# Kernel optimization log

Measured on AMD Instinct MI355X. Metric: run time of the kernel, lower is better.

## Reference

```python
import jax, jax.numpy as jnp
import numpy as np
from functools import partial

P = 14          # patch size
IMG = 448       # image size
D = 1152        # hidden dim
H = 16          # num heads
DH = D // H     # head dim = 72
I = 4304        # intermediate dim
L = 4           # num layers
N = (IMG // P) ** 2  # 1024 patches
EPS = 1e-6


def setup_inputs() -> dict:
    key = jax.random.key(0)
    ks = jax.random.split(key, 24)
    s = 0.02
    inp = {
        "images": jax.random.normal(ks[0], (2, 2, IMG, IMG, 3), jnp.float32),
        "conv_w": jax.random.normal(ks[1], (P, P, 3, D), jnp.float32) * s,
        "conv_b": jnp.zeros((D,), jnp.float32),
        "pos_emb": jax.random.normal(ks[2], (N, D), jnp.float32) * s,
        # per-layer stacked parameters, leading axis L
        "ln1_g": jnp.ones((L, D), jnp.float32),
        "ln1_b": jnp.zeros((L, D), jnp.float32),
        "Wq": jax.random.normal(ks[3], (L, D, D), jnp.float32) * s,
        "bq": jnp.zeros((L, D), jnp.float32),
        "Wk": jax.random.normal(ks[4], (L, D, D), jnp.float32) * s,
        "bk": jnp.zeros((L, D), jnp.float32),
        "Wv": jax.random.normal(ks[5], (L, D, D), jnp.float32) * s,
        "bv": jnp.zeros((L, D), jnp.float32),
        "Wo": jax.random.normal(ks[6], (L, D, D), jnp.float32) * s,
        "bo": jnp.zeros((L, D), jnp.float32),
        "ln2_g": jnp.ones((L, D), jnp.float32),
        "ln2_b": jnp.zeros((L, D), jnp.float32),
        "W1": jax.random.normal(ks[7], (L, D, I), jnp.float32) * s,
        "b1": jnp.zeros((L, I), jnp.float32),
        "W2": jax.random.normal(ks[8], (L, I, D), jnp.float32) * s,
        "b2": jnp.zeros((L, D), jnp.float32),
        "lnf_g": jnp.ones((D,), jnp.float32),
        "lnf_b": jnp.zeros((D,), jnp.float32),
    }
    return inp


def _layernorm(x, g, b):
    mu = jnp.mean(x, axis=-1, keepdims=True)
    var = jnp.var(x, axis=-1, keepdims=True)
    return (x - mu) * jax.lax.rsqrt(var + EPS) * g + b


def _encoder(images, conv_w, conv_b, pos_emb, ln1_g, ln1_b, Wq, bq, Wk, bk,
             Wv, bv, Wo, bo, ln2_g, ln2_b, W1, b1, W2, b2, lnf_g, lnf_b):
    B, T = images.shape[0], images.shape[1]
    x = images.reshape((B * T,) + images.shape[2:])  # [BT, IMG, IMG, 3]
    # patch embedding: Conv2D stride=kernel=patch, VALID
    x = jax.lax.conv_general_dilated(
        x, conv_w, window_strides=(P, P), padding='VALID',
        dimension_numbers=('NHWC', 'HWIO', 'NHWC')) + conv_b
    x = x.reshape(B * T, N, D) + pos_emb  # add position embedding

    scale = 1.0 / jnp.sqrt(jnp.asarray(DH, x.dtype))

    def block(x, p):
        (g1, b1_, wq, bq_, wk, bk_, wv, bv_, wo, bo_, g2, b2_,
         w1, bm1, w2, bm2) = p
        h = _layernorm(x, g1, b1_)
        q = (h @ wq + bq_).reshape(-1, N, H, DH).transpose(0, 2, 1, 3)
        k = (h @ wk + bk_).reshape(-1, N, H, DH).transpose(0, 2, 1, 3)
        v = (h @ wv + bv_).reshape(-1, N, H, DH).transpose(0, 2, 1, 3)
        scores = jnp.einsum('bhqd,bhkd->bhqk', q, k) * scale
        probs = jax.nn.softmax(scores, axis=-1)
        attn = jnp.einsum('bhqk,bhkd->bhqd', probs, v)
        attn = attn.transpose(0, 2, 1, 3).reshape(-1, N, D)
        x = x + (attn @ wo + bo_)
        h = _layernorm(x, g2, b2_)
        h = jax.nn.gelu(h @ w1 + bm1, approximate=True) @ w2 + bm2
        return x + h, None

    params = (ln1_g, ln1_b, Wq, bq, Wk, bk, Wv, bv, Wo, bo,
              ln2_g, ln2_b, W1, b1, W2, b2)
    x, _ = jax.lax.scan(block, x, params)
    x = _layernorm(x, lnf_g, lnf_b)
    return x.reshape(B, T, N, D)


def reference(images, conv_w, conv_b, pos_emb, ln1_g, ln1_b, Wq, bq, Wk, bk,
              Wv, bv, Wo, bo, ln2_g, ln2_b, W1, b1, W2, b2, lnf_g, lnf_b):
    return _encoder(images, conv_w, conv_b, pos_emb, ln1_g, ln1_b, Wq, bq,
                    Wk, bk, Wv, bv, Wo, bo, ln2_g, ln2_b, W1, b1, W2, b2,
                    lnf_g, lnf_b)
```

## Files before the change

kernel.cpp:

```cpp
#include <hip/hip_runtime.h>
#include <hip/hip_bf16.h>
#include <stdint.h>
#include <math.h>

typedef __hip_bfloat16 bf16;
typedef __attribute__((ext_vector_type(4))) float floatx4;
typedef __attribute__((ext_vector_type(8))) __bf16 bf16x8;

typedef __attribute__((address_space(1))) void gvoid_t;
typedef __attribute__((address_space(3))) void lvoid_t;

__device__ __forceinline__ void gl_lds16(const void* g, void* l){
  __builtin_amdgcn_global_load_lds((gvoid_t*)g, (lvoid_t*)l, 16, 0, 0);
}

__device__ __forceinline__ float gelu_f(float v){
  float u = 0.7978845608028654f*(v + 0.044715f*v*v*v);
  float e = __expf(2.0f*u);
  return v*(1.0f - 1.0f/(e+1.0f));
}

template<int MODE>
__global__ __launch_bounds__(256,4)
void gemm_bf16(const bf16* __restrict__ A, const bf16* __restrict__ BT,
               const float* __restrict__ bias, void* __restrict__ C,
               int N, int K, int kc, float qs)
{
  __shared__ bf16 As[128*32];
  __shared__ bf16 Bs[128*32];
  const int tid  = threadIdx.x;
  const int wave = tid>>6, lane = tid&63;
  const int quad = lane>>4, l16 = lane&15;
  const int m0 = blockIdx.y*128, n0 = blockIdx.x*128;
  const int s  = blockIdx.z;
  const int kb = s*kc;
  const int ke = min(K, kb + kc);
  const int wm = (wave&1)*64, wn = (wave>>1)*64;
  floatx4 acc[4][4] = {};
  const bf16* ag = A  + (size_t)(m0 + wave*32 + (lane>>2))*K + (lane&3)*8;
  const bf16* bg = BT + (size_t)(n0 + wave*32 + (lane>>2))*K + (lane&3)*8;
  bf16* asl = As + wave*1024;
  bf16* bsl = Bs + wave*1024;
  const size_t row16 = (size_t)16*K;
  for (int k0=kb; k0<ke; k0+=32){
    __syncthreads();
    gl_lds16(ag + k0,          asl);
    gl_lds16(ag + k0 + row16,  asl + 512);
    gl_lds16(bg + k0,          bsl);
    gl_lds16(bg + k0 + row16,  bsl + 512);
    __syncthreads();
    bf16x8 af[4], bfr[4];
#pragma unroll
    for (int i=0;i<4;i++) af[i]  = *(const bf16x8*)(As + (wm + i*16 + l16)*32 + quad*8);
#pragma unroll
    for (int j=0;j<4;j++) bfr[j] = *(const bf16x8*)(Bs + (wn + j*16 + l16)*32 + quad*8);
#pragma unroll
    for (int i=0;i<4;i++)
#pragma unroll
      for (int j=0;j<4;j++)
        acc[i][j] = __builtin_amdgcn_mfma_f32_16x16x32_bf16(af[i], bfr[j], acc[i][j], 0,0,0);
  }
  const float scale = (MODE==3 && n0<1152) ? qs : 1.0f;
#pragma unroll
  for (int i=0;i<4;i++){
    const int gr0 = m0 + wm + i*16 + quad*4;
#pragma unroll
    for (int j=0;j<4;j++){
      const int gc = n0 + wn + j*16 + l16;
      const float bv = (MODE!=4 || s==0) ? bias[gc] : 0.f;
#pragma unroll
      for (int r=0;r<4;r++){
        const int gr = gr0 + r;
        float v = acc[i][j][r] + bv;
        if constexpr (MODE==1) v = gelu_f(v);
        if constexpr (MODE==3) v *= scale;
        if constexpr (MODE==4){
          ((bf16*)C)[((size_t)s*4096 + gr)*N + gc] = __float2bfloat16(v);
        } else {
          ((bf16*)C)[(size_t)gr*N + gc] = __float2bfloat16(v);
        }
      }
    }
  }
}

template<int OUTF32, int WRITEX>
__global__ __launch_bounds__(256)
void ln_red(const float* __restrict__ base, unsigned bmask,
            const bf16* __restrict__ part, int ks,
            const float* __restrict__ g, const float* __restrict__ b,
            float* __restrict__ xw, void* __restrict__ out)
{
  const int row  = blockIdx.x*4 + (threadIdx.x>>6);
  const int lane = threadIdx.x & 63;
  const float2* br = (const float2*)base + (size_t)(row & bmask)*576;
  float2 v[9];
#pragma unroll
  for (int r=0;r<9;r++) v[r] = br[r*64+lane];
  for (int s=0;s<ks;s++){
    const __hip_bfloat162* pr = (const __hip_bfloat162*)part + ((size_t)s*4096 + row)*576;
#pragma unroll
    for (int r=0;r<9;r++){
      const float2 pv = __bfloat1622float2(pr[r*64+lane]);
      v[r].x += pv.x; v[r].y += pv.y;
    }
  }
  float sm=0.f, ss=0.f;
#pragma unroll
  for (int r=0;r<9;r++){
    sm += v[r].x + v[r].y;
    ss += v[r].x*v[r].x + v[r].y*v[r].y;
  }
#pragma unroll
  for (int m=1;m<64;m<<=1){ sm += __shfl_xor(sm,m,64); ss += __shfl_xor(ss,m,64); }
  const float mean = sm*(1.0f/1152.0f);
  const float rs = rsqrtf(ss*(1.0f/1152.0f) - mean*mean + 1e-6f);
  const float2* gr2 = (const float2*)g;
  const float2* br2 = (const float2*)b;
#pragma unroll
  for (int r=0;r<9;r++){
    const int c = r*64+lane;
    if constexpr (WRITEX) ((float2*)xw)[(size_t)row*576 + c] = v[r];
    const float2 gg = gr2[c], bb = br2[c];
    const float o0 = (v[r].x-mean)*rs*gg.x + bb.x;
    const float o1 = (v[r].y-mean)*rs*gg.y + bb.y;
    if constexpr (OUTF32){
      ((float2*)out)[(size_t)row*576 + c] = make_float2(o0, o1);
    } else {
      __hip_bfloat162 hv;
      hv.x = __float2bfloat16(o0); hv.y = __float2bfloat16(o1);
      ((__hip_bfloat162*)out)[(size_t)row*576 + c] = hv;
    }
  }
}

__global__ __launch_bounds__(256)
void im2col_kernel(const float* __restrict__ img, bf16* __restrict__ out)
{
  const int idx = blockIdx.x*256 + threadIdx.x;
  const int kk = idx % 608;
  const int rr = idx / 608;
  float v = 0.f;
  if (kk < 588){
    const int bt = rr >> 10, n = rr & 1023;
    const int py = n >> 5, px = n & 31;
    const int ph = kk / 42;
    const int rem = kk - ph*42;
    const int pw = rem / 3;
    const int c  = rem - pw*3;
    v = img[(((size_t)bt*448 + py*14 + ph)*448 + px*14 + pw)*3 + c];
  }
  out[idx] = __float2bfloat16(v);
}

__global__ __launch_bounds__(256)
void transpose_cvt(const float* __restrict__ in, bf16* __restrict__ out,
                   int K, int N, int Kp, int Np)
{
  __shared__ float tile[32][33];
  const int nt = blockIdx.x*32, kt = blockIdx.y*32;
  const int r = threadIdx.x>>5, c = threadIdx.x&31;
#pragma unroll
  for (int i=0;i<4;i++){
    const int k = kt + r + i*8, n = nt + c;
    tile[r+i*8][c] = (k<K && n<N) ? in[(size_t)k*N + n] : 0.f;
  }
  __syncthreads();
#pragma unroll
  for (int i=0;i<4;i++){
    const int n = nt + r + i*8, k = kt + c;
    out[(size_t)n*Kp + k] = __float2bfloat16(tile[c][r+i*8]);
  }
}

__global__ __launch_bounds__(256)
void pack_biases(const float* __restrict__ bq, const float* __restrict__ bk,
                 const float* __restrict__ bv, const float* __restrict__ b1,
                 int l, float* __restrict__ bqkv, float* __restrict__ b1p,
                 float4* __restrict__ zbuf)
{
  const int i = blockIdx.x*256 + threadIdx.x;
  if (i < 3456){
    float v;
    if (i < 1152)      v = bq[l*1152 + i];
    else if (i < 2304) v = bk[l*1152 + i - 1152];
    else               v = bv[l*1152 + i - 2304];
    bqkv[i] = v;
  }
  if (i < 4352) b1p[i] = (i < 4304) ? b1[l*4304 + i] : 0.f;
  if (i == 0) *zbuf = make_float4(0.f,0.f,0.f,0.f);
}

__global__ __launch_bounds__(256)
void transpose_v(const bf16* __restrict__ src, bf16* __restrict__ dst)
{
  __shared__ bf16 tile[128][73];
  const int nc = blockIdx.x, bh = blockIdx.y;
  const int bt = bh>>4, hh = bh&15;
  const bf16* s = src + ((size_t)bt*1024 + nc*128)*3456 + 2304 + hh*72;
  for (int e=threadIdx.x; e<128*72; e+=256){
    const int n = e/72, dh = e - n*72;
    tile[n][dh] = s[(size_t)n*3456 + dh];
  }
  __syncthreads();
  bf16* d = dst + (size_t)bh*80*1024 + nc*128;
  const bf16 z = __float2bfloat16(0.f);
  for (int e=threadIdx.x; e<80*128; e+=256){
    const int dh = e>>7, n = e&127;
    d[(size_t)dh*1024 + n] = (dh<72) ? tile[n][dh] : z;
  }
}

__global__ __launch_bounds__(256,2)
void attn_kernel(const bf16* __restrict__ qkv, const bf16* __restrict__ vb,
                 const float4* __restrict__ zbuf, bf16* __restrict__ outp)
{
  __shared__ bf16 Ks[128*96];
  __shared__ bf16 Vs[80*128];
  __shared__ bf16 Ps[64*128];
  const int tid = threadIdx.x, wave = tid>>6, lane = tid&63;
  const int quad = lane>>4, l16 = lane&15;
  const int bh = blockIdx.y, q0 = blockIdx.x*64;
  const int bt = bh>>4, hh = bh&15;
  const bf16* vg = vb + (size_t)bh*80*1024;
  bf16x8 af0{}, af1{}, af2{};
  {
    const bf16* qp = qkv + (size_t)(bt*1024 + q0 + wave*16 + l16)*3456 + hh*72 + quad*8;
    af0 = *(const bf16x8*)(qp);
    af1 = *(const bf16x8*)(qp+32);
    if (quad==0) af2 = *(const bf16x8*)(qp+64);
  }
  float mr[4], lr[4];
#pragma unroll
  for (int r=0;r<4;r++){ mr[r] = -3.0e38f; lr[r] = 0.f; }
  floatx4 oacc[5] = {};
  for (int kc=0;kc<8;kc++){
    __syncthreads();
    {
      const char* kcb = (const char*)(qkv + (size_t)(bt*1024 + kc*128)*3456 + 1152 + hh*72);
#pragma unroll
      for (int i=0;i<6;i++){
        const int u = (wave*6+i)*64 + lane;
        const int row = u/12;
        const int pp = u - row*12;
        const int c = (pp & 12) | ((pp & 3) ^ (row & 3));
        const void* src = (c<9) ? (const void*)(kcb + (size_t)row*6912 + c*16)
                                : (const void*)zbuf;
        gl_lds16(src, (char*)Ks + (size_t)(wave*6+i)*1024);
      }
#pragma unroll
      for (int i=0;i<5;i++){
        const int u = (wave*5+i)*64 + lane;
        const int row = u>>4;
        const int pp = u & 15;
        const int c = (pp & 8) | ((pp & 7) ^ (row & 7));
        gl_lds16((const char*)vg + (size_t)row*2048 + kc*256 + c*16,
                 (char*)Vs + (size_t)(wave*5+i)*1024);
      }
    }
    __syncthreads();
    floatx4 sc[8] = {};
    const int ksw = (quad ^ (l16&3))*8;
#pragma unroll
    for (int ct=0;ct<8;ct++){
      const bf16* kr = Ks + (ct*16+l16)*96 + ksw;
      sc[ct] = __builtin_amdgcn_mfma_f32_16x16x32_bf16(af0, *(const bf16x8*)(kr   ), sc[ct],0,0,0);
      sc[ct] = __builtin_amdgcn_mfma_f32_16x16x32_bf16(af1, *(const bf16x8*)(kr+32), sc[ct],0,0,0);
      sc[ct] = __builtin_amdgcn_mfma_f32_16x16x32_bf16(af2, *(const bf16x8*)(kr+64), sc[ct],0,0,0);
    }
    float cm[4];
#pragma unroll
    for (int r=0;r<4;r++){
      cm[r] = sc[0][r];
#pragma unroll
      for (int ct=1;ct<8;ct++) cm[r] = fmaxf(cm[r], sc[ct][r]);
    }
#pragma unroll
    for (int off=1; off<16; off<<=1)
#pragma unroll
      for (int r=0;r<4;r++) cm[r] = fmaxf(cm[r], __shfl_xor(cm[r], off, 64));
    float al[4], ls[4];
#pragma unroll
    for (int r=0;r<4;r++){
      const float mn = fmaxf(mr[r], cm[r]);
      al[r] = exp2f(mr[r]-mn);
      mr[r] = mn; ls[r] = 0.f;
    }
#pragma unroll
    for (int ct=0;ct<8;ct++){
#pragma unroll
      for (int r=0;r<4;r++){
        const float pv = exp2f(sc[ct][r]-mr[r]);
        ls[r] += pv;
        const int row = wave*16+quad*4+r;
        const int c = ct*2 + (l16>>3);
        const int pp = (c & 8) | ((c & 7) ^ (row & 7));
        Ps[row*128 + pp*8 + (l16&7)] = __float2bfloat16(pv);
      }
    }
#pragma unroll
    for (int off=1; off<16; off<<=1)
#pragma unroll
      for (int r=0;r<4;r++) ls[r] += __shfl_xor(ls[r], off, 64);
#pragma unroll
    for (int r=0;r<4;r++) lr[r] = lr[r]*al[r] + ls[r];
#pragma unroll
    for (int t=0;t<5;t++)
#pragma unroll
      for (int r=0;r<4;r++) oacc[t][r] *= al[r];
    __syncthreads();
#pragma unroll
    for (int ks=0;ks<4;ks++){
      const int c = ks*4 + quad;
      const int pp = (c & 8) | ((c & 7) ^ (l16 & 7));
      const bf16x8 pf = *(const bf16x8*)(Ps + (wave*16+l16)*128 + pp*8);
#pragma unroll
      for (int t=0;t<5;t++){
        const bf16x8 vf = *(const bf16x8*)(Vs + (t*16+l16)*128 + pp*8);
        oacc[t] = __builtin_amdgcn_mfma_f32_16x16x32_bf16(pf, vf, oacc[t],0,0,0);
      }
    }
  }
#pragma unroll
  for (int t=0;t<5;t++){
    const int dh = t*16+l16;
    if (dh < 72){
#pragma unroll
      for (int r=0;r<4;r++){
        const int q = wave*16 + quad*4 + r;
        const float v = oacc[t][r] / lr[r];
        outp[((size_t)bt*1024 + q0 + q)*1152 + hh*72 + dh] = __float2bfloat16(v);
      }
    }
  }
}

extern "C" void kernel_launch(void* const* d_in, const int* in_sizes, int n_in,
                              void* d_out, int out_size, void* d_ws, size_t ws_size,
                              hipStream_t stream)
{
  (void)in_sizes; (void)n_in; (void)out_size; (void)ws_size;
  const float* images = (const float*)d_in[0];
  const float* conv_w = (const float*)d_in[1];
  const float* conv_b = (const float*)d_in[2];
  const float* pos_emb= (const float*)d_in[3];
  const float* ln1_g  = (const float*)d_in[4];
  const float* ln1_b  = (const float*)d_in[5];
  const float* Wq     = (const float*)d_in[6];
  const float* bq     = (const float*)d_in[7];
  const float* Wk     = (const float*)d_in[8];
  const float* bk     = (const float*)d_in[9];
  const float* Wv     = (const float*)d_in[10];
  const float* bv     = (const float*)d_in[11];
  const float* Wo     = (const float*)d_in[12];
  const float* bo     = (const float*)d_in[13];
  const float* ln2_g  = (const float*)d_in[14];
  const float* ln2_b  = (const float*)d_in[15];
  const float* W1     = (const float*)d_in[16];
  const float* b1     = (const float*)d_in[17];
  const float* W2     = (const float*)d_in[18];
  const float* b2     = (const float*)d_in[19];
  const float* lnf_g  = (const float*)d_in[20];
  const float* lnf_b  = (const float*)d_in[21];

  char* p = (char*)d_ws;
  auto take = [&](size_t nbytes)->char*{ char* q = p; p += (nbytes + 255) & ~(size_t)255; return q; };
  float* xw   = (float*)take(4096ull*1152*4);
  bf16* hbuf  = (bf16*) take(4096ull*1152*2);
  bf16* h1    = (bf16*) take(4096ull*4352*2);
  bf16* qkvr  = h1;
  bf16* vbuf  = (bf16*) take(64ull*80*1024*2);
  bf16* imcol = vbuf;
  bf16* aout  = (bf16*) take(4096ull*1152*2);
  bf16* WqkvT = (bf16*) take(3456ull*1152*2);
  bf16* WoT   = (bf16*) take(1152ull*1152*2);
  bf16* W1T   = (bf16*) take(4352ull*1152*2);
  bf16* cwT   = W1T;
  bf16* W2T   = (bf16*) take(1152ull*4352*2);
  bf16* Ppart = (bf16*) take(4ull*4096*1152*2);
  float* bqkv = (float*)take(3456*4);
  float* b1p  = (float*)take(4352*4);
  float4* zbuf= (float4*)take(256);

  const float qscale = 1.4426950408889634f / sqrtf(72.0f);

  im2col_kernel<<<9728, 256, 0, stream>>>(images, imcol);
  transpose_cvt<<<dim3(36,19), 256, 0, stream>>>(conv_w, cwT, 588, 1152, 608, 1152);
  gemm_bf16<4><<<dim3(9,32,2), 256, 0, stream>>>(imcol, cwT, conv_b, Ppart, 1152, 608, 320, 0.f);

  for (int l=0;l<4;l++){
    transpose_cvt<<<dim3(36,36), 256, 0, stream>>>(Wq + (size_t)l*1152*1152, WqkvT,                1152,1152,1152,1152);
    transpose_cvt<<<dim3(36,36), 256, 0, stream>>>(Wk + (size_t)l*1152*1152, WqkvT + 1152ull*1152, 1152,1152,1152,1152);
    transpose_cvt<<<dim3(36,36), 256, 0, stream>>>(Wv + (size_t)l*1152*1152, WqkvT + 2304ull*1152, 1152,1152,1152,1152);
    transpose_cvt<<<dim3(36,36), 256, 0, stream>>>(Wo + (size_t)l*1152*1152, WoT, 1152,1152,1152,1152);
    transpose_cvt<<<dim3(136,36),256, 0, stream>>>(W1 + (size_t)l*1152*4304, W1T, 1152,4304,1152,4352);
    transpose_cvt<<<dim3(36,136),256, 0, stream>>>(W2 + (size_t)l*4304*1152, W2T, 4304,1152,4352,1152);
    pack_biases<<<17,256,0,stream>>>(bq,bk,bv,b1,l,bqkv,b1p,zbuf);

    if (l==0)
      ln_red<0,1><<<1024,256,0,stream>>>(pos_emb, 1023u, Ppart, 2, ln1_g, ln1_b, xw, hbuf);
    else
      ln_red<0,1><<<1024,256,0,stream>>>(xw, 4095u, Ppart, 4, ln1_g + l*1152, ln1_b + l*1152, xw, hbuf);

    gemm_bf16<3><<<dim3(27,32,1),256,0,stream>>>(hbuf, WqkvT, bqkv, qkvr, 3456, 1152, 1152, qscale);
    transpose_v<<<dim3(8,64),256,0,stream>>>(qkvr, vbuf);
    attn_kernel<<<dim3(16,64),256,0,stream>>>(qkvr, vbuf, zbuf, aout);
    gemm_bf16<4><<<dim3(9,32,3),256,0,stream>>>(aout, WoT, bo + l*1152, Ppart, 1152, 1152, 384, 0.f);
    ln_red<0,1><<<1024,256,0,stream>>>(xw, 4095u, Ppart, 3, ln2_g + l*1152, ln2_b + l*1152, xw, hbuf);

    gemm_bf16<1><<<dim3(34,32,1),256,0,stream>>>(hbuf, W1T, b1p, h1, 4352, 1152, 1152, 0.f);
    gemm_bf16<4><<<dim3(9,32,4),256,0,stream>>>(h1, W2T, b2 + l*1152, Ppart, 1152, 4352, 1088, 0.f);
  }
  ln_red<1,0><<<1024,256,0,stream>>>(xw, 4095u, Ppart, 4, lnf_g, lnf_b, nullptr, (float*)d_out);
}
```

Measured before the change: 1.770 ms.

## Double-buffer GEMM LDS tiles and remap workgroups for XCD locality

The GEMM kernel now uses two LDS buffers per operand. It prefetches the next K-slice with global_load_lds while running MFMAs on the current one, which removes one barrier per iteration and overlaps memory with compute. Both the GEMM and attention kernels remap the flat workgroup id so that consecutive logical tiles land on the same XCD and are grouped along M, with the aim of improving L2 reuse. The costs are doubled LDS per block, which could limit occupancy, and remapping formulas that assume grid sizes divisible by eight and a fixed attention grid shape.

After: 1.625 ms. -8.2%, faster.

```diff
diff --git a/kernel.cpp b/kernel.cpp
--- a/kernel.cpp
+++ b/kernel.cpp
@@ -26,12 +26,28 @@
                const float* __restrict__ bias, void* __restrict__ C,
                int N, int K, int kc, float qs)
 {
-  __shared__ bf16 As[128*32];
-  __shared__ bf16 Bs[128*32];
+  __shared__ bf16 As[2][128*32];
+  __shared__ bf16 Bs[2][128*32];
   const int tid  = threadIdx.x;
   const int wave = tid>>6, lane = tid&63;
   const int quad = lane>>4, l16 = lane&15;
-  const int m0 = blockIdx.y*128, n0 = blockIdx.x*128;
+
+  int bm, bn;
+  {
+    const int nx = gridDim.x;
+    const int nwg = nx * gridDim.y;
+    int lid = blockIdx.x + nx*blockIdx.y;
+    const int q = nwg >> 3, r = nwg & 7;
+    const int xcd = lid & 7, off = lid >> 3;
+    lid = (xcd < r ? xcd*(q+1) : r*(q+1) + (xcd - r)*q) + off;
+    const int per = nx << 3;
+    const int g   = lid / per;
+    const int rem = lid - g*per;
+    bm = (g<<3) + (rem & 7);
+    bn = rem >> 3;
+  }
+  const int m0 = bm*128, n0 = bn*128;
+
   const int s  = blockIdx.z;
   const int kb = s*kc;
   const int ke = min(K, kb + kc);
@@ -39,26 +55,37 @@
   floatx4 acc[4][4] = {};
   const bf16* ag = A  + (size_t)(m0 + wave*32 + (lane>>2))*K + (lane&3)*8;
   const bf16* bg = BT + (size_t)(n0 + wave*32 + (lane>>2))*K + (lane&3)*8;
-  bf16* asl = As + wave*1024;
-  bf16* bsl = Bs + wave*1024;
   const size_t row16 = (size_t)16*K;
+  const int woff = wave*1024;
+
+  gl_lds16(ag + kb,          As[0] + woff);
+  gl_lds16(ag + kb + row16,  As[0] + woff + 512);
+  gl_lds16(bg + kb,          Bs[0] + woff);
+  gl_lds16(bg + kb + row16,  Bs[0] + woff + 512);
+
+  int cur = 0;
   for (int k0=kb; k0<ke; k0+=32){
     __syncthreads();
-    gl_lds16(ag + k0,          asl);
-    gl_lds16(ag + k0 + row16,  asl + 512);
-    gl_lds16(bg + k0,          bsl);
-    gl_lds16(bg + k0 + row16,  bsl + 512);
-    __syncthreads();
+    const int kn = k0 + 32;
+    if (kn < ke){
+      bf16* asn = As[cur^1] + woff;
+      bf16* bsn = Bs[cur^1] + woff;
+      gl_lds16(ag + kn,          asn);
+      gl_lds16(ag + kn + row16,  asn + 512);
+      gl_lds16(bg + kn,          bsn);
+      gl_lds16(bg + kn + row16,  bsn + 512);
+    }
     bf16x8 af[4], bfr[4];
 #pragma unroll
-    for (int i=0;i<4;i++) af[i]  = *(const bf16x8*)(As + (wm + i*16 + l16)*32 + quad*8);
-#pragma unroll
-    for (int j=0;j<4;j++) bfr[j] = *(const bf16x8*)(Bs + (wn + j*16 + l16)*32 + quad*8);
+    for (int i=0;i<4;i++) af[i]  = *(const bf16x8*)(As[cur] + (wm + i*16 + l16)*32 + quad*8);
+#pragma unroll
+    for (int j=0;j<4;j++) bfr[j] = *(const bf16x8*)(Bs[cur] + (wn + j*16 + l16)*32 + quad*8);
 #pragma unroll
     for (int i=0;i<4;i++)
 #pragma unroll
       for (int j=0;j<4;j++)
         acc[i][j] = __builtin_amdgcn_mfma_f32_16x16x32_bf16(af[i], bfr[j], acc[i][j], 0,0,0);
+    cur ^= 1;
   }
   const float scale = (MODE==3 && n0<1152) ? qs : 1.0f;
 #pragma unroll
@@ -220,7 +247,9 @@
   __shared__ bf16 Ps[64*128];
   const int tid = threadIdx.x, wave = tid>>6, lane = tid&63;
   const int quad = lane>>4, l16 = lane&15;
-  const int bh = blockIdx.y, q0 = blockIdx.x*64;
+  int lid = blockIdx.x + (blockIdx.y<<4);
+  lid = ((lid & 7) << 7) + (lid >> 3);
+  const int bh = lid >> 4, q0 = (lid & 15) << 6;
   const int bt = bh>>4, hh = bh&15;
   const bf16* vg = vb + (size_t)bh*80*1024;
   bf16x8 af0{}, af1{}, af2{};
```
